# Performance work log

Hardware: AMD Instinct MI355X
Metric: run time of the kernel (lower is better)

Reference implementation:

```python
import jax, jax.numpy as jnp
import numpy as np

D = 512      # node_feature_size
LAT = 768    # latent_size
B = 16       # number of graphs
S = 256      # conditioning sequence length
H = 8        # attention heads


def _ln(x, g, b):
    m = x.mean(-1, keepdims=True)
    v = jnp.var(x, axis=-1, keepdims=True)
    return (x - m) / jnp.sqrt(v + 1e-5) * g + b


def setup_inputs() -> dict:
    key = jax.random.key(0)
    ks = jax.random.split(key, 10)
    lengths = np.array([512 + 32 * i for i in range(B)])  # ragged node counts
    N = int(lengths.sum())                                # 12032
    Lmax = int(lengths.max())                             # 992
    graph_batch = jnp.asarray(np.repeat(np.arange(B), lengths), dtype=jnp.int32)
    valid = np.array([S - 8 * i for i in range(B)])
    # torch key_padding_mask semantics: True = position is ignored (padding)
    conditioning_mask = jnp.asarray(np.arange(S)[None, :] >= valid[:, None])
    p = lambda k, sh: jax.random.normal(k, sh, jnp.float32) * 0.02
    return dict(
        graph_nodes=jax.random.normal(ks[0], (N, D), jnp.float32),
        graph_batch=graph_batch,
        conditioning_vector=jax.random.normal(ks[1], (B, S, LAT), jnp.float32),
        conditioning_mask=conditioning_mask,
        max_nodes=Lmax,
        num_heads=H,
        Wq=p(ks[2], (D, D)), bq=jnp.zeros(D, jnp.float32),
        Wk=p(ks[3], (LAT, D)), bk=jnp.zeros(D, jnp.float32),
        Wv=p(ks[4], (LAT, D)), bv=jnp.zeros(D, jnp.float32),
        in_w=p(ks[5], (3, D, D)), in_b=jnp.zeros((3, D), jnp.float32),
        Wo=p(ks[6], (D, D)), bo=jnp.zeros(D, jnp.float32),
        ln1_g=jnp.ones(D, jnp.float32), ln1_b=jnp.zeros(D, jnp.float32),
        W1=p(ks[7], (D, D)), b1=jnp.zeros(D, jnp.float32),
        ln2_g=jnp.ones(D, jnp.float32), ln2_b=jnp.zeros(D, jnp.float32),
    )


def reference(graph_nodes, graph_batch, conditioning_vector, conditioning_mask,
              max_nodes, num_heads, Wq, bq, Wk, bk, Wv, bv, in_w, in_b,
              Wo, bo, ln1_g, ln1_b, W1, b1, ln2_g, ln2_b):
    N, Dm = graph_nodes.shape
    Bn, Sk, _ = conditioning_vector.shape
    dh = Dm // num_heads
    # --- pad ragged node sets to dense [B, Lmax, D] (vectorized scatter) ---
    counts = jax.ops.segment_sum(jnp.ones(N, jnp.int32), graph_batch, num_segments=Bn)
    starts = jnp.concatenate([jnp.zeros(1, jnp.int32), jnp.cumsum(counts)[:-1].astype(jnp.int32)])
    pos = jnp.arange(N, dtype=jnp.int32) - starts[graph_batch]
    dense = jnp.zeros((Bn, max_nodes, Dm), graph_nodes.dtype).at[graph_batch, pos].set(graph_nodes)
    # --- projections ---
    q = dense @ Wq + bq
    k = conditioning_vector @ Wk + bk
    v = conditioning_vector @ Wv + bv
    # --- MultiheadAttention internal in-projections ---
    qh = (q @ in_w[0] + in_b[0]).reshape(Bn, max_nodes, num_heads, dh)
    kh = (k @ in_w[1] + in_b[1]).reshape(Bn, Sk, num_heads, dh)
    vh = (v @ in_w[2] + in_b[2]).reshape(Bn, Sk, num_heads, dh)
    scores = jnp.einsum('blhd,bshd->bhls', qh, kh) / jnp.sqrt(jnp.asarray(dh, qh.dtype))
    scores = jnp.where(conditioning_mask[:, None, None, :], -jnp.inf, scores)
    attn = jax.nn.softmax(scores, axis=-1)     # [B,H,L,S]
    av_attn = attn.mean(axis=1)                # head-averaged weights [B,L,S]
    ctx = jnp.einsum('bhls,bshd->blhd', attn, vh).reshape(Bn, max_nodes, Dm)
    attn_out = ctx @ Wo + bo
    # --- residual + LN + FFN + LN (dropout inactive / eval mode) ---
    x = _ln(attn_out + dense, ln1_g, ln1_b)
    x = jax.nn.leaky_relu(x @ W1 + b1) + x     # slope 0.01 matches nn.LeakyReLU
    x = _ln(x, ln2_g, ln2_b)
    # --- unpad back to ragged [N, D] (vectorized gather) ---
    node_out = x[graph_batch, pos]
    return node_out, av_attn
```

## Files before the change

### kernel.cpp

```cpp
#include <hip/hip_runtime.h>
#include <math.h>

#define D_   512
#define LAT_ 768
#define B_   16
#define S_   256
#define H_   8
#define DH_  64

typedef __bf16 bf16x8 __attribute__((ext_vector_type(8)));
typedef float f32x4 __attribute__((ext_vector_type(4)));

__device__ __forceinline__ unsigned short f2bf(float f) {
  unsigned u = __float_as_uint(f);
  unsigned r = (u + 0x7fffu + ((u >> 16) & 1u)) >> 16;
  return (unsigned short)r;
}

__global__ void prep_k(const void* __restrict__ mask, int* __restrict__ maskc,
                       const int* __restrict__ gb, int* __restrict__ starts, int n) {
  int i = blockIdx.x * blockDim.x + threadIdx.x;
  if (i < B_ * S_) {
    const unsigned char* pb = (const unsigned char*)mask;
    const int*   pi = (const int*)mask;
    const float* pf = (const float*)mask;
    unsigned int w = ((const unsigned int*)mask)[1023];
    int v;
    if (w == 0x01010101u)      v = pb[i];
    else if (w == 0x3f800000u) v = (pf[i] != 0.0f);
    else                       v = (pi[i] != 0);
    maskc[i] = v ? 1 : 0;
  }
  if (i < n) {
    if (i == 0 || gb[i] != gb[i - 1]) starts[gb[i]] = i;
  }
}

__global__ __launch_bounds__(256) void scatter_k(const float* __restrict__ nodes,
    const int* __restrict__ gb, const int* __restrict__ starts,
    float* __restrict__ dense, int Lmax) {
  int i = blockIdx.x;
  int b = gb[i], p = i - starts[b];
  const float* src = nodes + (size_t)i * D_;
  float* dst = dense + ((size_t)b * Lmax + p) * D_;
  dst[threadIdx.x]       = src[threadIdx.x];
  dst[threadIdx.x + 256] = src[threadIdx.x + 256];
}

__device__ __forceinline__ void pack_chunk(const float* __restrict__ W,
    unsigned short* __restrict__ out, int K, int ntoff, int idx) {
  int n = idx & 511, kc = idx >> 9;
  int kt = kc >> 2, kblk = kc & 3;
  int nt = n >> 7, nblk = (n >> 4) & 7, col = n & 15;
  int KT = K >> 5;
  size_t ob = ((size_t)((nt + ntoff) * KT + kt) * 4096) + nblk * 512 + kblk * 128 + col * 8;
  unsigned short v[8];
#pragma unroll
  for (int j = 0; j < 8; ++j) v[j] = f2bf(W[(size_t)(kc * 8 + j) * 512 + n]);
  int4 pk;
  pk.x = v[0] | (v[1] << 16); pk.y = v[2] | (v[3] << 16);
  pk.z = v[4] | (v[5] << 16); pk.w = v[6] | (v[7] << 16);
  *(int4*)&out[ob] = pk;
}

__global__ __launch_bounds__(256) void pack1_k(const float* __restrict__ in_w,
    const float* __restrict__ Wo, const float* __restrict__ W1,
    unsigned short* iw0, unsigned short* iw1, unsigned short* iw2,
    unsigned short* Wo_pk, unsigned short* W1_pk) {
  int bid = blockIdx.x, sel = bid >> 7, within = bid & 127;
  const float* W; unsigned short* out;
  switch (sel) {
    case 0: W = in_w;               out = iw0;   break;
    case 1: W = in_w + 512 * 512;   out = iw1;   break;
    case 2: W = in_w + 2 * 512 * 512; out = iw2; break;
    case 3: W = Wo;                 out = Wo_pk; break;
    default: W = W1;                out = W1_pk; break;
  }
  pack_chunk(W, out, 512, 0, within * 256 + threadIdx.x);
}

__global__ __launch_bounds__(256) void pack2_k(const float* __restrict__ Wqp,
    const float* __restrict__ Wkp, const float* __restrict__ Wvp,
    unsigned short* Wqp_pk, unsigned short* kv_pk) {
  int bid = blockIdx.x, tid = threadIdx.x;
  if (bid < 128)      pack_chunk(Wqp, Wqp_pk, 512, 0, bid * 256 + tid);
  else if (bid < 320) pack_chunk(Wkp, kv_pk, 768, 0, (bid - 128) * 256 + tid);
  else                pack_chunk(Wvp, kv_pk, 768, 4, (bid - 320) * 256 + tid);
}

__device__ __forceinline__ void mgemm64(const float* __restrict__ A,
    const unsigned short* __restrict__ Bpk, const float* __restrict__ bias,
    float* __restrict__ C, __bf16* __restrict__ Cb,
    int M, int N, int K, int xt, int yt,
    unsigned short* Al, unsigned short* Bl) {
  const int tid = threadIdx.x;
  const int lane = tid & 63, wid = tid >> 6;
  const int wr = wid >> 1, wc = wid & 1;
  const int row0 = yt * 64, col0 = xt * 128;
  const int KT32 = K >> 5;
  const int NIT = K >> 6;
  f32x4 acc[2][4];
#pragma unroll
  for (int m = 0; m < 2; ++m)
#pragma unroll
    for (int n = 0; n < 4; ++n) acc[m][n] = (f32x4){0.f, 0.f, 0.f, 0.f};
  const int kb0 = tid & 3, ar = tid >> 2;
  const unsigned short* bsrc = Bpk + (size_t)xt * KT32 * 4096;

  for (int it = 0; it < NIT; ++it) {
#pragma unroll
    for (int j = 0; j < 4; ++j) {
      size_t off = (size_t)(2 * it + (j >> 1)) * 4096 + (j & 1) * 2048 + wid * 512 + lane * 8;
      size_t doff = (size_t)(j >> 1) * 4096 + (j & 1) * 2048 + wid * 512 + lane * 8;
      __builtin_amdgcn_global_load_lds(
          (const __attribute__((address_space(1))) void*)(bsrc + off),
          (__attribute__((address_space(3))) void*)&Bl[doff], 16, 0, 0);
    }
#pragma unroll
    for (int hh = 0; hh < 2; ++hh) {
      const float* ap = A + (size_t)(row0 + ar) * K + it * 64 + hh * 32 + kb0 * 8;
      float4 f0 = *(const float4*)ap;
      float4 f1 = *(const float4*)(ap + 4);
      int4 pk;
      pk.x = f2bf(f0.x) | (f2bf(f0.y) << 16);
      pk.y = f2bf(f0.z) | (f2bf(f0.w) << 16);
      pk.z = f2bf(f1.x) | (f2bf(f1.y) << 16);
      pk.w = f2bf(f1.z) | (f2bf(f1.w) << 16);
      *(int4*)&Al[hh * 2048 + (ar >> 4) * 512 + kb0 * 128 + (ar & 15) * 8] = pk;
    }
    __syncthreads();
#pragma unroll
    for (int hh = 0; hh < 2; ++hh) {
      bf16x8 af[2], bfr[4];
#pragma unroll
      for (int m = 0; m < 2; ++m)
        af[m] = *(const bf16x8*)&Al[hh * 2048 + (wr * 2 + m) * 512 + lane * 8];
#pragma unroll
      for (int n = 0; n < 4; ++n)
        bfr[n] = *(const bf16x8*)&Bl[hh * 4096 + (wc * 4 + n) * 512 + lane * 8];
#pragma unroll
      for (int m = 0; m < 2; ++m)
#pragma unroll
        for (int n = 0; n < 4; ++n)
          acc[m][n] = __builtin_amdgcn_mfma_f32_16x16x32_bf16(af[m], bfr[n], acc[m][n], 0, 0, 0);
    }
    __syncthreads();
  }
  const int cl = lane & 15, rg = lane >> 4;
  float bv[4];
#pragma unroll
  for (int n = 0; n < 4; ++n)
    bv[n] = bias ? bias[col0 + wc * 64 + n * 16 + cl] : 0.f;
#pragma unroll
  for (int m = 0; m < 2; ++m) {
    int r = row0 + wr * 32 + m * 16 + rg * 4;
#pragma unroll
    for (int n = 0; n < 4; ++n) {
      int c = col0 + wc * 64 + n * 16 + cl;
#pragma unroll
      for (int i = 0; i < 4; ++i) {
        float v = acc[m][n][i] + bv[n];
        if (Cb) Cb[(size_t)(r + i) * N + c] = (__bf16)v;
        else    C[(size_t)(r + i) * N + c] = v;
      }
    }
  }
}

__global__ __launch_bounds__(256) void gemm64_k(const float* __restrict__ A,
    const unsigned short* __restrict__ Bpk, const float* __restrict__ bias,
    float* __restrict__ C, int M, int N, int K) {
  __shared__ __align__(16) unsigned short Al[4096];
  __shared__ __align__(16) unsigned short Bl[8192];
  mgemm64(A, Bpk, bias, C, nullptr, M, N, K, blockIdx.x, blockIdx.y, Al, Bl);
}

__global__ __launch_bounds__(256) void fold_k(const float* __restrict__ Wq,
    const float* __restrict__ Wk, const float* __restrict__ Wv,
    const unsigned short* iw0, const unsigned short* iw1, const unsigned short* iw2,
    float* Wqp, float* Wkp, float* Wvp) {
  __shared__ __align__(16) unsigned short Al[4096];
  __shared__ __align__(16) unsigned short Bl[8192];
  int bid = blockIdx.x;
  if (bid < 32)       mgemm64(Wq, iw0, nullptr, Wqp, nullptr, 512, 512, 512, bid & 3, bid >> 2, Al, Bl);
  else if (bid < 80)  { int r = bid - 32; mgemm64(Wk, iw1, nullptr, Wkp, nullptr, 768, 512, 512, r & 3, r >> 2, Al, Bl); }
  else                { int r = bid - 80; mgemm64(Wv, iw2, nullptr, Wvp, nullptr, 768, 512, 512, r & 3, r >> 2, Al, Bl); }
}

__global__ __launch_bounds__(256) void proj_k(const float* __restrict__ dense,
    const float* __restrict__ cond, const unsigned short* Wqp_pk,
    const unsigned short* kv_pk, const float* __restrict__ bqp,
    const float* __restrict__ bkv, float* qh, __bf16* kvh, int BL) {
  __shared__ __align__(16) unsigned short Al[4096];
  __shared__ __align__(16) unsigned short Bl[8192];
  int bid = blockIdx.x;
  int nq = (BL >> 6) << 2;
  if (bid < nq)
    mgemm64(dense, Wqp_pk, bqp, qh, nullptr, BL, 512, 512, bid & 3, bid >> 2, Al, Bl);
  else {
    int r = bid - nq;
    mgemm64(cond, kv_pk, bkv, nullptr, kvh, B_ * S_, 1024, LAT_, r & 7, r >> 3, Al, Bl);
  }
}

__global__ void bias3_k(const float* __restrict__ bq, const float* __restrict__ bk,
    const float* __restrict__ bv, const float* __restrict__ in_w,
    const float* __restrict__ in_b, float* bqp, float* bkv) {
  int sel = blockIdx.x >> 1;
  int j = (blockIdx.x & 1) * 256 + threadIdx.x;
  const float* bin; const float* W; const float* badd; float* out;
  if (sel == 0)      { bin = bq; W = in_w;                 badd = in_b;          out = bqp; }
  else if (sel == 1) { bin = bk; W = in_w + 512 * 512;     badd = in_b + D_;     out = bkv; }
  else               { bin = bv; W = in_w + 2 * 512 * 512; badd = in_b + 2 * D_; out = bkv + 512; }
  float s = badd[j];
  for (int k = 0; k < D_; ++k) s += bin[k] * W[(size_t)k * D_ + j];
  out[j] = s;
}

__device__ __forceinline__ float rmax16(float v) {
  v = fmaxf(v, __shfl_xor(v, 1)); v = fmaxf(v, __shfl_xor(v, 2));
  v = fmaxf(v, __shfl_xor(v, 4)); v = fmaxf(v, __shfl_xor(v, 8));
  return v;
}
__device__ __forceinline__ float rsum16(float v) {
  v += __shfl_xor(v, 1); v += __shfl_xor(v, 2);
  v += __shfl_xor(v, 4); v += __shfl_xor(v, 8);
  return v;
}

__global__ __launch_bounds__(256) void attn_k(const float* __restrict__ qh,
    const __bf16* __restrict__ kvh, const int* __restrict__ maskc,
    float* __restrict__ ctx, float* __restrict__ avout, int Lmax) {
  const int bid = blockIdx.x;
  const int b = bid & 15;
  const int l0 = (bid >> 4) * 32;
  const int tid = threadIdx.x;
  const int lane = tid & 63, w = tid >> 6;
  const int lg = lane >> 4, l15 = lane & 15;
  __shared__ __align__(16) __bf16 v_lds[256][68];
  __shared__ __align__(16) __bf16 p_lds[32][260];
  __shared__ float maxred[4][32];
  __shared__ float sumred[4][32];
  float madd[4];
#pragma unroll
  for (int n = 0; n < 4; ++n)
    madd[n] = maskc[b * S_ + w * 64 + n * 16 + l15] ? -1.0e30f : 0.f;

  float av[2][4][4];
#pragma unroll
  for (int m = 0; m < 2; ++m)
#pragma unroll
    for (int n = 0; n < 4; ++n)
#pragma unroll
      for (int i = 0; i < 4; ++i) av[m][n][i] = 0.f;

  const size_t qrow0 = (size_t)b * Lmax + l0;
  const int srow = tid >> 2, scol = (tid & 3) * 16;

#pragma unroll 1
  for (int h = 0; h < H_; ++h) {
    __syncthreads();
#pragma unroll
    for (int pass = 0; pass < 4; ++pass) {
      int s = pass * 64 + srow;
      const __bf16* vp = kvh + (size_t)(b * S_ + s) * 1024 + 512 + h * DH_ + scol;
      *(bf16x8*)&v_lds[s][scol]     = *(const bf16x8*)vp;
      *(bf16x8*)&v_lds[s][scol + 8] = *(const bf16x8*)(vp + 8);
    }
    f32x4 qk[2][4];
#pragma unroll
    for (int m = 0; m < 2; ++m)
#pragma unroll
      for (int n = 0; n < 4; ++n) qk[m][n] = (f32x4){0.f, 0.f, 0.f, 0.f};
#pragma unroll
    for (int kt = 0; kt < 2; ++kt) {
      bf16x8 afr[2];
#pragma unroll
      for (int m = 0; m < 2; ++m) {
        const float* qp = qh + (qrow0 + m * 16 + l15) * D_ + h * DH_ + kt * 32 + lg * 8;
        float4 f0 = *(const float4*)qp, f1 = *(const float4*)(qp + 4);
        afr[m][0] = (__bf16)f0.x; afr[m][1] = (__bf16)f0.y;
        afr[m][2] = (__bf16)f0.z; afr[m][3] = (__bf16)f0.w;
        afr[m][4] = (__bf16)f1.x; afr[m][5] = (__bf16)f1.y;
        afr[m][6] = (__bf16)f1.z; afr[m][7] = (__bf16)f1.w;
      }
#pragma unroll
      for (int n = 0; n < 4; ++n) {
        const __bf16* kp = kvh + ((size_t)(b * S_) + w * 64 + n * 16 + l15) * 1024
                           + h * DH_ + kt * 32 + lg * 8;
        bf16x8 bfr = *(const bf16x8*)kp;
#pragma unroll
        for (int m = 0; m < 2; ++m)
          qk[m][n] = __builtin_amdgcn_mfma_f32_16x16x32_bf16(afr[m], bfr, qk[m][n], 0, 0, 0);
      }
    }
#pragma unroll
    for (int m = 0; m < 2; ++m)
#pragma unroll
      for (int n = 0; n < 4; ++n)
#pragma unroll
        for (int i = 0; i < 4; ++i)
          qk[m][n][i] = qk[m][n][i] * 0.125f + madd[n];
    float pm[2][4];
#pragma unroll
    for (int m = 0; m < 2; ++m)
#pragma unroll
      for (int i = 0; i < 4; ++i) {
        float v = fmaxf(fmaxf(qk[m][0][i], qk[m][1][i]), fmaxf(qk[m][2][i], qk[m][3][i]));
        pm[m][i] = rmax16(v);
      }
    if (l15 == 0) {
#pragma unroll
      for (int m = 0; m < 2; ++m)
#pragma unroll
        for (int i = 0; i < 4; ++i) maxred[w][m * 16 + lg * 4 + i] = pm[m][i];
    }
    __syncthreads();
    float gm[2][4], ps[2][4];
#pragma unroll
    for (int m = 0; m < 2; ++m)
#pragma unroll
      for (int i = 0; i < 4; ++i) {
        int row = m * 16 + lg * 4 + i;
        gm[m][i] = fmaxf(fmaxf(maxred[0][row], maxred[1][row]),
                         fmaxf(maxred[2][row], maxred[3][row]));
        ps[m][i] = 0.f;
      }
#pragma unroll
    for (int m = 0; m < 2; ++m)
#pragma unroll
      for (int n = 0; n < 4; ++n)
#pragma unroll
        for (int i = 0; i < 4; ++i) {
          float e = __expf(qk[m][n][i] - gm[m][i]);
          qk[m][n][i] = e;
          ps[m][i] += e;
        }
#pragma unroll
    for (int m = 0; m < 2; ++m)
#pragma unroll
      for (int i = 0; i < 4; ++i) pm[m][i] = rsum16(ps[m][i]);
    if (l15 == 0) {
#pragma unroll
      for (int m = 0; m < 2; ++m)
#pragma unroll
        for (int i = 0; i < 4; ++i) sumred[w][m * 16 + lg * 4 + i] = pm[m][i];
    }
    __syncthreads();
#pragma unroll
    for (int m = 0; m < 2; ++m)
#pragma unroll
      for (int i = 0; i < 4; ++i) {
        int row = m * 16 + lg * 4 + i;
        float inv = 1.f / (sumred[0][row] + sumred[1][row] + sumred[2][row] + sumred[3][row]);
#pragma unroll
        for (int n = 0; n < 4; ++n) {
          float p = qk[m][n][i] * inv;
          av[m][n][i] += p * 0.125f;
          p_lds[row][w * 64 + n * 16 + l15] = (__bf16)p;
        }
      }
    __syncthreads();
    f32x4 pv[2];
    pv[0] = (f32x4){0.f, 0.f, 0.f, 0.f};
    pv[1] = (f32x4){0.f, 0.f, 0.f, 0.f};
#pragma unroll
    for (int ks = 0; ks < 8; ++ks) {
      bf16x8 vb;
#pragma unroll
      for (int j = 0; j < 8; ++j) vb[j] = v_lds[ks * 32 + lg * 8 + j][w * 16 + l15];
#pragma unroll
      for (int m = 0; m < 2; ++m) {
        bf16x8 pa = *(const bf16x8*)&p_lds[m * 16 + l15][ks * 32 + lg * 8];
        pv[m] = __builtin_amdgcn_mfma_f32_16x16x32_bf16(pa, vb, pv[m], 0, 0, 0);
      }
    }
#pragma unroll
    for (int m = 0; m < 2; ++m)
#pragma unroll
      for (int i = 0; i < 4; ++i)
        ctx[(qrow0 + m * 16 + lg * 4 + i) * D_ + h * DH_ + w * 16 + l15] = pv[m][i];
  }
#pragma unroll
  for (int m = 0; m < 2; ++m)
#pragma unroll
    for (int i = 0; i < 4; ++i) {
      size_t arow = (qrow0 + m * 16 + lg * 4 + i) * S_;
#pragma unroll
      for (int n = 0; n < 4; ++n)
        avout[arow + w * 64 + n * 16 + l15] = av[m][n][i];
    }
}

__global__ __launch_bounds__(256) void ln_add_k(const float* __restrict__ a,
    const float* __restrict__ r, const float* __restrict__ g,
    const float* __restrict__ be, float* __restrict__ out) {
  const int wv = threadIdx.x >> 6, lane = threadIdx.x & 63;
  const size_t row = ((size_t)blockIdx.x * 4 + wv) * D_;
  const int c0 = lane * 8;
  float4 a0 = *(const float4*)(a + row + c0);
  float4 a1 = *(const float4*)(a + row + c0 + 4);
  float4 r0 = *(const float4*)(r + row + c0);
  float4 r1 = *(const float4*)(r + row + c0 + 4);
  float v[8] = {a0.x + r0.x, a0.y + r0.y, a0.z + r0.z, a0.w + r0.w,
                a1.x + r1.x, a1.y + r1.y, a1.z + r1.z, a1.w + r1.w};
  float s = 0.f, sq = 0.f;
#pragma unroll
  for (int j = 0; j < 8; ++j) { s += v[j]; sq += v[j] * v[j]; }
#pragma unroll
  for (int off = 1; off < 64; off <<= 1) {
    s  += __shfl_xor(s, off);
    sq += __shfl_xor(sq, off);
  }
  float mean = s * (1.f / D_);
  float var  = sq * (1.f / D_) - mean * mean;
  float rstd = rsqrtf(var + 1e-5f);
  float4 o0, o1;
  o0.x = (v[0] - mean) * rstd * g[c0 + 0] + be[c0 + 0];
  o0.y = (v[1] - mean) * rstd * g[c0 + 1] + be[c0 + 1];
  o0.z = (v[2] - mean) * rstd * g[c0 + 2] + be[c0 + 2];
  o0.w = (v[3] - mean) * rstd * g[c0 + 3] + be[c0 + 3];
  o1.x = (v[4] - mean) * rstd * g[c0 + 4] + be[c0 + 4];
  o1.y = (v[5] - mean) * rstd * g[c0 + 5] + be[c0 + 5];
  o1.z = (v[6] - mean) * rstd * g[c0 + 6] + be[c0 + 6];
  o1.w = (v[7] - mean) * rstd * g[c0 + 7] + be[c0 + 7];
  *(float4*)(out + row + c0)     = o0;
  *(float4*)(out + row + c0 + 4) = o1;
}

__global__ __launch_bounds__(256) void final_k(const float* __restrict__ h1,
    const float* __restrict__ x1, const int* __restrict__ gb,
    const int* __restrict__ starts, const float* __restrict__ g,
    const float* __restrict__ be, float* __restrict__ out, int Lmax) {
  const int wv = threadIdx.x >> 6, lane = threadIdx.x & 63;
  const int i = blockIdx.x * 4 + wv;
  const int b = gb[i], p = i - starts[b];
  const size_t row = ((size_t)b * Lmax + p) * D_;
  const int c0 = lane * 8;
  float4 h0 = *(const float4*)(h1 + row + c0);
  float4 h4 = *(const float4*)(h1 + row + c0 + 4);
  float4 x0 = *(const float4*)(x1 + row + c0);
  float4 x4 = *(const float4*)(x1 + row + c0 + 4);
  float v[8] = {h0.x, h0.y, h0.z, h0.w, h4.x, h4.y, h4.z, h4.w};
  float xr[8] = {x0.x, x0.y, x0.z, x0.w, x4.x, x4.y, x4.z, x4.w};
  float s = 0.f, sq = 0.f;
#pragma unroll
  for (int j = 0; j < 8; ++j) {
    float t = v[j];
    t = (t >= 0.f) ? t : 0.01f * t;
    t += xr[j];
    v[j] = t;
    s += t; sq += t * t;
  }
#pragma unroll
  for (int off = 1; off < 64; off <<= 1) {
    s  += __shfl_xor(s, off);
    sq += __shfl_xor(sq, off);
  }
  float mean = s * (1.f / D_);
  float var  = sq * (1.f / D_) - mean * mean;
  float rstd = rsqrtf(var + 1e-5f);
  float4 o0, o1;
  o0.x = (v[0] - mean) * rstd * g[c0 + 0] + be[c0 + 0];
  o0.y = (v[1] - mean) * rstd * g[c0 + 1] + be[c0 + 1];
  o0.z = (v[2] - mean) * rstd * g[c0 + 2] + be[c0 + 2];
  o0.w = (v[3] - mean) * rstd * g[c0 + 3] + be[c0 + 3];
  o1.x = (v[4] - mean) * rstd * g[c0 + 4] + be[c0 + 4];
  o1.y = (v[5] - mean) * rstd * g[c0 + 5] + be[c0 + 5];
  o1.z = (v[6] - mean) * rstd * g[c0 + 6] + be[c0 + 6];
  o1.w = (v[7] - mean) * rstd * g[c0 + 7] + be[c0 + 7];
  *(float4*)(out + (size_t)i * D_ + c0)     = o0;
  *(float4*)(out + (size_t)i * D_ + c0 + 4) = o1;
}

extern "C" void kernel_launch(void* const* d_in, const int* in_sizes, int n_in,
                              void* d_out, int out_size, void* d_ws, size_t ws_size,
                              hipStream_t stream) {
  const float* nodes = (const float*)d_in[0];
  const int*   gb    = (const int*)d_in[1];
  const float* cond  = (const float*)d_in[2];
  const void*  maskp = d_in[3];
  const float* Wq   = (const float*)d_in[6];
  const float* bq   = (const float*)d_in[7];
  const float* Wk   = (const float*)d_in[8];
  const float* bk   = (const float*)d_in[9];
  const float* Wv   = (const float*)d_in[10];
  const float* bv   = (const float*)d_in[11];
  const float* in_w = (const float*)d_in[12];
  const float* in_b = (const float*)d_in[13];
  const float* Wo   = (const float*)d_in[14];
  const float* bo   = (const float*)d_in[15];
  const float* g1   = (const float*)d_in[16];
  const float* b1ln = (const float*)d_in[17];
  const float* W1   = (const float*)d_in[18];
  const float* b1f  = (const float*)d_in[19];
  const float* g2   = (const float*)d_in[20];
  const float* b2ln = (const float*)d_in[21];

  const int N    = in_sizes[0] / D_;
  const int Lmax = (out_size - N * D_) / (B_ * S_);
  const int BL   = B_ * Lmax;

  float* ws = (float*)d_ws;
  int* starts = (int*)(ws + 0);
  int* maskc  = (int*)(ws + 64);
  size_t o = 8192;
  float* dense = ws + o; o += (size_t)BL * D_;
  float* qh    = ws + o; o += (size_t)BL * D_;
  float* ctx   = qh;
  __bf16* kvh  = (__bf16*)(ws + o); o += (size_t)B_ * S_ * 1024 / 2;
  float* tmp   = ws + o; o += (size_t)BL * D_;
  float* x1    = ws + o; o += (size_t)BL * D_;
  float* h1    = dense;
  float* Wqp = ws + o; o += (size_t)D_ * D_;
  float* Wkp = ws + o; o += (size_t)LAT_ * D_;
  float* Wvp = ws + o; o += (size_t)LAT_ * D_;
  float* bqp = ws + o; o += D_;
  float* bkv = ws + o; o += 1024;
  unsigned short* iw0_pk = (unsigned short*)(ws + o); o += (size_t)D_ * D_ / 2;
  unsigned short* iw1_pk = (unsigned short*)(ws + o); o += (size_t)D_ * D_ / 2;
  unsigned short* iw2_pk = (unsigned short*)(ws + o); o += (size_t)D_ * D_ / 2;
  unsigned short* Wqp_pk = (unsigned short*)(ws + o); o += (size_t)D_ * D_ / 2;
  unsigned short* kv_pk  = (unsigned short*)(ws + o); o += (size_t)LAT_ * 1024 / 2;
  unsigned short* Wo_pk  = (unsigned short*)(ws + o); o += (size_t)D_ * D_ / 2;
  unsigned short* W1_pk  = (unsigned short*)(ws + o); o += (size_t)D_ * D_ / 2;

  (void)hipMemsetAsync(d_ws, 0, (8192 + (size_t)BL * D_) * sizeof(float), stream);

  prep_k<<<(N + 255) / 256, 256, 0, stream>>>(maskp, maskc, gb, starts, N);
  scatter_k<<<N, 256, 0, stream>>>(nodes, gb, starts, dense, Lmax);

  pack1_k<<<640, 256, 0, stream>>>(in_w, Wo, W1, iw0_pk, iw1_pk, iw2_pk, Wo_pk, W1_pk);
  fold_k<<<128, 256, 0, stream>>>(Wq, Wk, Wv, iw0_pk, iw1_pk, iw2_pk, Wqp, Wkp, Wvp);
  pack2_k<<<512, 256, 0, stream>>>(Wqp, Wkp, Wvp, Wqp_pk, kv_pk);
  bias3_k<<<6, 256, 0, stream>>>(bq, bk, bv, in_w, in_b, bqp, bkv);

  proj_k<<<(BL >> 6) * 4 + 512, 256, 0, stream>>>(dense, cond, Wqp_pk, kv_pk,
      bqp, bkv, qh, kvh, BL);

  attn_k<<<(Lmax / 32) * B_, 256, 0, stream>>>(qh, kvh, maskc, ctx,
      (float*)d_out + (size_t)N * D_, Lmax);

  gemm64_k<<<dim3(4, BL / 64), 256, 0, stream>>>(ctx, Wo_pk, bo, tmp, BL, D_, D_);
  ln_add_k<<<BL / 4, 256, 0, stream>>>(tmp, dense, g1, b1ln, x1);

  gemm64_k<<<dim3(4, BL / 64), 256, 0, stream>>>(x1, W1_pk, b1f, h1, BL, D_, D_);
  final_k<<<N / 4, 256, 0, stream>>>(h1, x1, gb, starts, g2, b2ln, (float*)d_out, Lmax);
}
```

Baseline: 248.6 us.

## Split attention heads across two block groups and merge averaged weights

The attention kernel grid is doubled so that each block processes four of the eight heads instead of all eight, writing partial head-averaged weights into two buffers. A new merge kernel then adds the two partial buffers into the output. This gives more blocks, and so more parallelism, on a grid that was previously only 496 blocks. The cost is an extra kernel launch, an extra global buffer, and additional read/write traffic for the averaged-weight tensor. The block-to-group split is hardcoded at 496, which assumes Lmax=992.

After: 258.6 us. 4.0% more time.

```diff
diff --git a/kernel.cpp b/kernel.cpp
--- a/kernel.cpp
+++ b/kernel.cpp
@@ -230,10 +230,13 @@
 
 __global__ __launch_bounds__(256) void attn_k(const float* __restrict__ qh,
     const __bf16* __restrict__ kvh, const int* __restrict__ maskc,
-    float* __restrict__ ctx, float* __restrict__ avout, int Lmax) {
+    float* __restrict__ ctx, float* __restrict__ av0,
+    float* __restrict__ av1, int Lmax) {
   const int bid = blockIdx.x;
-  const int b = bid & 15;
-  const int l0 = (bid >> 4) * 32;
+  const int grp = (bid >= 496) ? 1 : 0;
+  const int r0i = bid - grp * 496;
+  const int b = r0i & 15;
+  const int l0 = (r0i >> 4) * 32;
   const int tid = threadIdx.x;
   const int lane = tid & 63, w = tid >> 6;
   const int lg = lane >> 4, l15 = lane & 15;
@@ -256,9 +259,10 @@
 
   const size_t qrow0 = (size_t)b * Lmax + l0;
   const int srow = tid >> 2, scol = (tid & 3) * 16;
+  const int h0 = grp * 4;
 
 #pragma unroll 1
-  for (int h = 0; h < H_; ++h) {
+  for (int h = h0; h < h0 + 4; ++h) {
     __syncthreads();
 #pragma unroll
     for (int pass = 0; pass < 4; ++pass) {
@@ -381,6 +385,7 @@
       for (int i = 0; i < 4; ++i)
         ctx[(qrow0 + m * 16 + lg * 4 + i) * D_ + h * DH_ + w * 16 + l15] = pv[m][i];
   }
+  float* avp = grp ? av1 : av0;
 #pragma unroll
   for (int m = 0; m < 2; ++m)
 #pragma unroll
@@ -388,8 +393,17 @@
       size_t arow = (qrow0 + m * 16 + lg * 4 + i) * S_;
 #pragma unroll
       for (int n = 0; n < 4; ++n)
-        avout[arow + w * 64 + n * 16 + l15] = av[m][n][i];
-    }
+        avp[arow + w * 64 + n * 16 + l15] = av[m][n][i];
+    }
+}
+
+__global__ __launch_bounds__(256) void avmerge_k(float* __restrict__ avout,
+    const float* __restrict__ av1) {
+  size_t i = ((size_t)blockIdx.x * 256 + threadIdx.x) * 4;
+  float4 a = *(const float4*)(avout + i);
+  float4 c = *(const float4*)(av1 + i);
+  a.x += c.x; a.y += c.y; a.z += c.z; a.w += c.w;
+  *(float4*)(avout + i) = a;
 }
 
 __global__ __launch_bounds__(256) void ln_add_k(const float* __restrict__ a,
@@ -512,6 +526,7 @@
   float* tmp   = ws + o; o += (size_t)BL * D_;
   float* x1    = ws + o; o += (size_t)BL * D_;
   float* h1    = dense;
+  float* av1   = ws + o; o += (size_t)BL * S_;
   float* Wqp = ws + o; o += (size_t)D_ * D_;
   float* Wkp = ws + o; o += (size_t)LAT_ * D_;
   float* Wvp = ws + o; o += (size_t)LAT_ * D_;
@@ -538,8 +553,10 @@
   proj_k<<<(BL >> 6) * 4 + 512, 256, 0, stream>>>(dense, cond, Wqp_pk, kv_pk,
       bqp, bkv, qh, kvh, BL);
 
-  attn_k<<<(Lmax / 32) * B_, 256, 0, stream>>>(qh, kvh, maskc, ctx,
-      (float*)d_out + (size_t)N * D_, Lmax);
+  float* avout = (float*)d_out + (size_t)N * D_;
+  attn_k<<<(Lmax / 32) * B_ * 2, 256, 0, stream>>>(qh, kvh, maskc, ctx,
+      avout, av1, Lmax);
+  avmerge_k<<<(BL * S_ / 4) / 256, 256, 0, stream>>>(avout, av1);
 
   gemm64_k<<<dim3(4, BL / 64), 256, 0, stream>>>(ctx, Wo_pk, bo, tmp, BL, D_, D_);
   ln_add_k<<<BL / 4, 256, 0, stream>>>(tmp, dense, g1, b1ln, x1);
```
